# Kernel tuning notes

Measured on AMD Instinct MI355X. Metric: run time of the kernel, lower is better.

The kernel has to match this reference:

```python
import jax, jax.numpy as jnp
import numpy as np

NUM_CLASSES = 80
NUM_ANCHORS = 5
STRIDE = 32
THRESH = 0.6
MAX_BOXES = 50
ANCHORS = np.array([[42.0, 55.0], [102.0, 128.0], [161.0, 259.0],
                    [303.0, 155.0], [359.0, 320.0]], dtype=np.float32)
SCALED_ANCHORS = jnp.asarray(ANCHORS / STRIDE)  # [nA, 2] in grid units


def _bce_sum(p, t):
    # torch nn.BCELoss(reduction='sum') with log clamped at -100
    lp = jnp.clip(jnp.log(p), -100.0, None)
    l1p = jnp.clip(jnp.log1p(-p), -100.0, None)
    return -jnp.sum(t * lp + (1.0 - t) * l1p)


def _build_targets(target, nH, nW):
    """Vectorized port of build_targets_yolov2 (one scatter per tensor)."""
    nA, nC, T = NUM_ANCHORS, NUM_CLASSES, MAX_BOXES
    nB = target.shape[0]
    tg = target.reshape(nB, T, 5)  # (class, x, y, w, h)
    # loop breaks at first x==0 -> cumulative validity along box dim
    valid = jnp.cumprod((tg[:, :, 1] != 0.0).astype(jnp.int32), axis=1).astype(bool)
    gx = tg[..., 1] * nW
    gy = tg[..., 2] * nH
    gw = tg[..., 3] * nW
    gh = tg[..., 4] * nH
    gi = jnp.clip(gx.astype(jnp.int32), 0, nW - 1)
    gj = jnp.clip(gy.astype(jnp.int32), 0, nH - 1)
    aw = SCALED_ANCHORS[:, 0]
    ah = SCALED_ANCHORS[:, 1]
    # IoU of (0,0,gw,gh) vs (0,0,aw,ah) with the original's +1 convention
    inter = (jnp.maximum(jnp.minimum(gw[..., None], aw) + 1.0, 0.0)
             * jnp.maximum(jnp.minimum(gh[..., None], ah) + 1.0, 0.0))
    ious = inter / ((gw[..., None] + 1.0) * (gh[..., None] + 1.0)
                    + (aw + 1.0) * (ah + 1.0) - inter + 1e-16)  # [nB, T, nA]
    best = jnp.argmax(ious, axis=-1)  # [nB, T]
    b_idx = jnp.broadcast_to(jnp.arange(nB)[:, None], (nB, T))
    vf = valid.astype(jnp.float32)
    # noobj cleared where iou > thresh at (gj, gi), and always at the best anchor
    clear = ((ious > THRESH) | (jnp.arange(nA)[None, None, :] == best[..., None])) & valid[..., None]
    bb = jnp.broadcast_to(b_idx[..., None], (nB, T, nA))
    aa = jnp.broadcast_to(jnp.arange(nA)[None, None, :], (nB, T, nA))
    jj = jnp.broadcast_to(gj[..., None], (nB, T, nA))
    ii = jnp.broadcast_to(gi[..., None], (nB, T, nA))
    clear_grid = jnp.zeros((nB, nA, nH, nW)).at[bb, aa, jj, ii].max(clear.astype(jnp.float32))
    noobj = 1.0 - clear_grid
    obj = jnp.zeros((nB, nA, nH, nW)).at[b_idx, best, gj, gi].max(vf)

    def scat(vals):
        return jnp.zeros((nB, nA, nH, nW)).at[b_idx, best, gj, gi].set(jnp.where(valid, vals, 0.0))

    tx = scat(gx - gi.astype(gx.dtype))
    ty = scat(gy - gj.astype(gy.dtype))
    tw = scat(jnp.log(jnp.maximum(gw, 1e-8) / aw[best]))
    th = scat(jnp.log(jnp.maximum(gh, 1e-8) / ah[best]))
    tconf = obj
    cls = jnp.clip(tg[..., 0].astype(jnp.int32), 0, nC - 1)
    tcls = jnp.zeros((nB, nA, nH, nW, nC)).at[b_idx, best, gj, gi, cls].max(vf)
    return obj, noobj, tx, ty, tw, th, tconf, tcls


def setup_inputs() -> dict:
    key = jax.random.key(0)
    k1, k2, k3, k4 = jax.random.split(key, 4)
    nB, nH, nW = 64, 32, 32
    output = jax.random.normal(k1, (nB, NUM_ANCHORS * (5 + NUM_CLASSES), nH, nW), dtype=jnp.float32)
    # structured targets: (class, x, y, w, h), x in (0,1) so all 50 boxes valid
    cls = jax.random.randint(k2, (nB, MAX_BOXES, 1), 0, NUM_CLASSES).astype(jnp.float32)
    xy = jax.random.uniform(k3, (nB, MAX_BOXES, 2), minval=0.02, maxval=0.98)
    wh = jax.random.uniform(k4, (nB, MAX_BOXES, 2), minval=0.05, maxval=0.6)
    target = jnp.concatenate([cls, xy, wh], axis=-1).reshape(nB, MAX_BOXES * 5)
    return {"output": output, "target": target}


def reference(output, target):
    nB, _, nH, nW = output.shape
    nA, nC = NUM_ANCHORS, NUM_CLASSES
    out = output.reshape(nB, nA, 5 + nC, nH, nW).transpose(0, 1, 3, 4, 2)  # [nB,nA,nH,nW,5+nC]
    x = jax.nn.sigmoid(out[..., 0])
    y = jax.nn.sigmoid(out[..., 1])
    w = out[..., 2]
    h = out[..., 3]
    pred_conf = jax.nn.sigmoid(out[..., 4])
    pred_cls = jax.nn.sigmoid(out[..., 5:])
    tgt = jax.lax.stop_gradient(target)  # torch uses target.data
    obj, noobj, tx, ty, tw, th, tconf, tcls = _build_targets(tgt, nH, nW)
    loss_x = _bce_sum(x * obj, tx * obj)
    loss_y = _bce_sum(y * obj, ty * obj)
    loss_w = jnp.sum((w * obj - tw * obj) ** 2)
    loss_h = jnp.sum((h * obj - th * obj) ** 2)
    loss_conf = _bce_sum(pred_conf * obj, obj) + 0.5 * _bce_sum(pred_conf * noobj, jnp.zeros_like(pred_conf))
    # pred_cls[obj==1] BCE-sum == elementwise BCE masked by obj
    lp = jnp.clip(jnp.log(pred_cls), -100.0, None)
    l1p = jnp.clip(jnp.log1p(-pred_cls), -100.0, None)
    bce_cls = -(tcls * lp + (1.0 - tcls) * l1p)
    loss_cls = jnp.sum(bce_cls * obj[..., None])
    return (loss_x + loss_y + loss_w + loss_h + loss_conf + loss_cls) / nB
```

## Files before the change

kernel.cpp:

```cpp
#include <hip/hip_runtime.h>
#include <math.h>

#define NCLS 80
#define NA 5
#define NH 32
#define NW 32
#define TBX 50
#define CH (5 + NCLS)
#define QPIX 256

__device__ __forceinline__ float sigm(float z) { return 1.0f / (1.0f + expf(-z)); }

__device__ __forceinline__ float bce(float p, float t) {
    float lp  = fmaxf(logf(p), -100.0f);
    float l1p = fmaxf(log1pf(-p), -100.0f);
    return -(t * lp + (1.0f - t) * l1p);
}

__global__ __launch_bounds__(256) void yolo_loss_kernel(
    const float* __restrict__ outp, const float* __restrict__ target,
    float* __restrict__ partials)
{
    const int blk = blockIdx.x;
    const int q   = blk & 3;
    const int bA  = blk >> 2;
    const int b   = bA / NA;
    const int A   = bA - b * NA;
    const int tid = threadIdx.x;

    const float* base = outp + ((size_t)b * (NA * CH) + (size_t)A * CH) * (NH * NW)
                        + (size_t)q * QPIX;
    const float conf = base[4 * 1024 + tid];

    __shared__ float s_tx[TBX], s_ty[TBX], s_tw[TBX], s_th[TBX];
    __shared__ unsigned char s_valid[TBX];
    __shared__ int      winner[QPIX];
    __shared__ unsigned clsm[QPIX][3];
    __shared__ unsigned clearbits[QPIX / 32];
    __shared__ unsigned objbits[QPIX / 32];
    __shared__ int   objlist[TBX];
    __shared__ float s_part[4];

    winner[tid] = -1;
    clsm[tid][0] = 0; clsm[tid][1] = 0; clsm[tid][2] = 0;
    if (tid < QPIX / 32) { clearbits[tid] = 0; objbits[tid] = 0; }

    const bool active = tid < TBX;
    int  cell = 0, cls = 0;
    bool match = false, clearb = false, v = false;
    if (active) {
        const float* tg = target + (size_t)b * TBX * 5 + tid * 5;
        float clsf = tg[0];
        float xx = tg[1], yy = tg[2], ww = tg[3], hh = tg[4];
        float gx = xx * NW, gy = yy * NH, gw = ww * NW, gh = hh * NH;
        int gi = (int)gx; gi = min(max(gi, 0), NW - 1);
        int gj = (int)gy; gj = min(max(gj, 0), NH - 1);
        const float AW[NA] = {1.3125f, 3.1875f, 5.03125f, 9.46875f, 11.21875f};
        const float AH[NA] = {1.71875f, 4.0f,   8.09375f, 4.84375f, 10.0f};
        int best = 0; float bi = -1.0f, bw = 0.f, bh = 0.f, iouA = 0.f;
        #pragma unroll
        for (int a = 0; a < NA; ++a) {
            float aw = AW[a], ah = AH[a];
            float inter = fmaxf(fminf(gw, aw) + 1.0f, 0.0f) * fmaxf(fminf(gh, ah) + 1.0f, 0.0f);
            float iou = inter / ((gw + 1.0f) * (gh + 1.0f) + (aw + 1.0f) * (ah + 1.0f) - inter + 1e-16f);
            if (iou > bi) { bi = iou; best = a; bw = aw; bh = ah; }
            if (a == A) iouA = iou;
        }
        cell   = gj * NW + gi;
        match  = (best == A);
        clearb = (iouA > 0.6f) || match;
        cls = (int)clsf; cls = min(max(cls, 0), NCLS - 1);
        unsigned long long m = __ballot(xx != 0.0f);
        v = (((~m) & ((1ULL << (tid + 1)) - 1ULL)) == 0ULL);
        s_valid[tid] = v ? 1 : 0;
        s_tx[tid] = gx - (float)gi;
        s_ty[tid] = gy - (float)gj;
        s_tw[tid] = logf(fmaxf(gw, 1e-8f) / bw);
        s_th[tid] = logf(fmaxf(gh, 1e-8f) / bh);
    }
    __syncthreads();

    if (active && (cell >> 8) == q) {
        int p = cell & (QPIX - 1);
        if (clearb && v) atomicOr(&clearbits[p >> 5], 1u << (p & 31));
        if (match) {
            atomicMax(&winner[p], tid);
            if (v) {
                atomicOr(&objbits[p >> 5], 1u << (p & 31));
                atomicOr(&clsm[p][cls >> 5], 1u << (cls & 31));
            }
        }
    }
    __syncthreads();

    float lsum = 0.0f;
    const int p = tid;
    const unsigned ow = objbits[p >> 5];
    const unsigned objb = (ow >> (p & 31)) & 1u;
    const unsigned clrb = (clearbits[p >> 5] >> (p & 31)) & 1u;
    if (objb) {
        int rank = __popc(ow & ((1u << (p & 31)) - 1u));
        for (int k = 0; k < (p >> 5); ++k) rank += __popc(objbits[k]);
        objlist[rank] = p;
    } else if (!clrb) {
        lsum += -0.5f * fmaxf(log1pf(-sigm(conf)), -100.0f);
    }
    int nobj = 0;
    #pragma unroll
    for (int k = 0; k < QPIX / 32; ++k) nobj += __popc(objbits[k]);
    __syncthreads();

    const int total = nobj * CH;
    for (int idx = tid; idx < total; idx += 256) {
        int e = idx / CH;
        int c = idx - e * CH;
        int pc = objlist[e];
        float oc = base[c * 1024 + pc];
        int w = winner[pc];
        bool wv = s_valid[w] != 0;
        float contrib;
        if (c == 0)      contrib = bce(sigm(oc), wv ? s_tx[w] : 0.0f);
        else if (c == 1) contrib = bce(sigm(oc), wv ? s_ty[w] : 0.0f);
        else if (c == 2) { float d = oc - (wv ? s_tw[w] : 0.0f); contrib = d * d; }
        else if (c == 3) { float d = oc - (wv ? s_th[w] : 0.0f); contrib = d * d; }
        else if (c == 4) contrib = -fmaxf(logf(sigm(oc)), -100.0f);
        else {
            int cc = c - 5;
            unsigned bit = (clsm[pc][cc >> 5] >> (cc & 31)) & 1u;
            contrib = bce(sigm(oc), bit ? 1.0f : 0.0f);
        }
        lsum += contrib;
    }

    #pragma unroll
    for (int off = 32; off > 0; off >>= 1)
        lsum += __shfl_down(lsum, off, 64);
    if ((tid & 63) == 0) s_part[tid >> 6] = lsum;
    __syncthreads();
    if (tid == 0)
        partials[blk] = s_part[0] + s_part[1] + s_part[2] + s_part[3];
}

__global__ __launch_bounds__(256) void reduce_kernel(
    const float* __restrict__ partials, float* __restrict__ out,
    int n, float inv_nB)
{
    const int tid = threadIdx.x;
    float s = 0.0f;
    for (int i = tid; i < n; i += 256) s += partials[i];
    #pragma unroll
    for (int off = 32; off > 0; off >>= 1)
        s += __shfl_down(s, off, 64);
    __shared__ float sp[4];
    if ((tid & 63) == 0) sp[tid >> 6] = s;
    __syncthreads();
    if (tid == 0)
        out[0] = (sp[0] + sp[1] + sp[2] + sp[3]) * inv_nB;
}

extern "C" void kernel_launch(void* const* d_in, const int* in_sizes, int n_in,
                              void* d_out, int out_size, void* d_ws, size_t ws_size,
                              hipStream_t stream) {
    const float* outp   = (const float*)d_in[0];
    const float* target = (const float*)d_in[1];
    float* loss = (float*)d_out;
    float* partials = (float*)d_ws;
    int nB = in_sizes[1] / (TBX * 5);
    int nblk = nB * NA * 4;
    yolo_loss_kernel<<<nblk, 256, 0, stream>>>(outp, target, partials);
    reduce_kernel<<<1, 256, 0, stream>>>(partials, loss, nblk, 1.0f / (float)nB);
}
```

Baseline: 19.46 us.

## Fuse final reduction into main kernel via hierarchical last-block atomic counters

Measured after the change: 63.57 us. +226.7%, slower.

```diff
diff --git a/kernel.cpp b/kernel.cpp
--- a/kernel.cpp
+++ b/kernel.cpp
@@ -8,6 +8,7 @@
 #define TBX 50
 #define CH (5 + NCLS)
 #define QPIX 256
+#define NGRP 16
 
 __device__ __forceinline__ float sigm(float z) { return 1.0f / (1.0f + expf(-z)); }
 
@@ -19,7 +20,11 @@
 
 __global__ __launch_bounds__(256) void yolo_loss_kernel(
     const float* __restrict__ outp, const float* __restrict__ target,
-    float* __restrict__ partials)
+    float* __restrict__ partials,
+    unsigned long long* __restrict__ grpctr,
+    unsigned long long* __restrict__ rootctr,
+    float* __restrict__ out,
+    int nblk, float inv_nB)
 {
     const int blk = blockIdx.x;
     const int q   = blk & 3;
@@ -40,6 +45,7 @@
     __shared__ unsigned objbits[QPIX / 32];
     __shared__ int   objlist[TBX];
     __shared__ float s_part[4];
+    __shared__ int   s_trigger;
 
     winner[tid] = -1;
     clsm[tid][0] = 0; clsm[tid][1] = 0; clsm[tid][2] = 0;
@@ -137,25 +143,39 @@
         lsum += __shfl_down(lsum, off, 64);
     if ((tid & 63) == 0) s_part[tid >> 6] = lsum;
     __syncthreads();
-    if (tid == 0)
-        partials[blk] = s_part[0] + s_part[1] + s_part[2] + s_part[3];
-}
 
-__global__ __launch_bounds__(256) void reduce_kernel(
-    const float* __restrict__ partials, float* __restrict__ out,
-    int n, float inv_nB)
-{
-    const int tid = threadIdx.x;
-    float s = 0.0f;
-    for (int i = tid; i < n; i += 256) s += partials[i];
-    #pragma unroll
-    for (int off = 32; off > 0; off >>= 1)
-        s += __shfl_down(s, off, 64);
-    __shared__ float sp[4];
-    if ((tid & 63) == 0) sp[tid >> 6] = s;
+    if (tid == 0) {
+        float part = s_part[0] + s_part[1] + s_part[2] + s_part[3];
+        __hip_atomic_store(&partials[blk], part, __ATOMIC_RELAXED, __HIP_MEMORY_SCOPE_AGENT);
+        __threadfence();
+        int g = blk & (NGRP - 1);
+        unsigned long long quota =
+            (unsigned long long)(nblk / NGRP + (g < (nblk % NGRP) ? 1 : 0));
+        int trig = 0;
+        unsigned long long old = __hip_atomic_fetch_add(
+            &grpctr[g * 8], 1ULL, __ATOMIC_ACQ_REL, __HIP_MEMORY_SCOPE_AGENT);
+        if (old % quota == quota - 1ULL) {
+            unsigned long long r = __hip_atomic_fetch_add(
+                rootctr, 1ULL, __ATOMIC_ACQ_REL, __HIP_MEMORY_SCOPE_AGENT);
+            if (r % NGRP == NGRP - 1ULL) trig = 1;
+        }
+        s_trigger = trig;
+    }
     __syncthreads();
-    if (tid == 0)
-        out[0] = (sp[0] + sp[1] + sp[2] + sp[3]) * inv_nB;
+
+    if (s_trigger) {
+        __threadfence();
+        float s = 0.0f;
+        for (int i = tid; i < nblk; i += 256)
+            s += __hip_atomic_load(&partials[i], __ATOMIC_RELAXED, __HIP_MEMORY_SCOPE_AGENT);
+        #pragma unroll
+        for (int off = 32; off > 0; off >>= 1)
+            s += __shfl_down(s, off, 64);
+        if ((tid & 63) == 0) s_part[tid >> 6] = s;
+        __syncthreads();
+        if (tid == 0)
+            out[0] = (s_part[0] + s_part[1] + s_part[2] + s_part[3]) * inv_nB;
+    }
 }
 
 extern "C" void kernel_launch(void* const* d_in, const int* in_sizes, int n_in,
@@ -164,9 +184,15 @@
     const float* outp   = (const float*)d_in[0];
     const float* target = (const float*)d_in[1];
     float* loss = (float*)d_out;
-    float* partials = (float*)d_ws;
     int nB = in_sizes[1] / (TBX * 5);
     int nblk = nB * NA * 4;
-    yolo_loss_kernel<<<nblk, 256, 0, stream>>>(outp, target, partials);
-    reduce_kernel<<<1, 256, 0, stream>>>(partials, loss, nblk, 1.0f / (float)nB);
+
+    char* ws = (char*)d_ws;
+    float* partials = (float*)ws;
+    size_t off = ((size_t)nblk * sizeof(float) + 63) & ~(size_t)63;
+    unsigned long long* grpctr  = (unsigned long long*)(ws + off);
+    unsigned long long* rootctr = (unsigned long long*)(ws + off + NGRP * 64);
+
+    yolo_loss_kernel<<<nblk, 256, 0, stream>>>(
+        outp, target, partials, grpctr, rootctr, loss, nblk, 1.0f / (float)nB);
 }
```
